# Kernel optimization log

Measured on AMD Instinct MI355X. Metric: run time of the kernel, lower is better.

Reference implementation:

```python
import jax, jax.numpy as jnp
import numpy as np

H = 32        # num query heads
KVH = 8       # num kv heads
D = 128       # head_dim
ROPE_BASE = 10000.0
NEG_INF = jnp.finfo(jnp.float32).min


def rope_interleaved(x):
    """Interleaved (GPT-NeoX-style pairs (x0,x1),(x2,x3),...) RoPE. x: [b,s,h,d]."""
    d = x.shape[-1]
    inv_freq = 1.0 / (ROPE_BASE ** (jnp.arange(0, d, 2, dtype=jnp.float32) / d))  # [d/2]
    pos = jnp.arange(x.shape[1], dtype=jnp.float32)
    ang = pos[:, None] * inv_freq[None, :]                    # [s, d/2]
    cos = jnp.cos(ang)[None, :, None, :]
    sin = jnp.sin(ang)[None, :, None, :]
    xp = x.reshape(*x.shape[:-1], d // 2, 2)
    x1, x2 = xp[..., 0], xp[..., 1]
    r1 = x1 * cos - x2 * sin
    r2 = x1 * sin + x2 * cos
    return jnp.stack([r1, r2], axis=-1).reshape(x.shape)


def setup_inputs() -> dict:
    key = jax.random.key(0)
    k1, k2, k3 = jax.random.split(key, 3)
    B, S, E = 2, 2048, 4096
    x = jax.random.normal(k1, (B, S, E), dtype=jnp.float32)
    wqkv = jax.random.normal(k2, (E + 2 * KVH * D, E), dtype=jnp.float32) * 0.02
    wo = jax.random.normal(k3, (E, E), dtype=jnp.float32) * 0.02
    return {"x": x, "wqkv": wqkv, "wo": wo}


def reference(x, wqkv, wo):
    b, s, e = x.shape
    q_per_kv = H // KVH
    # fused QKV projection (torch Linear layout: y = x @ W.T)
    qkv = jnp.einsum('bse,fe->bsf', x, wqkv)
    # rearrange 'b s (h gs d) -> b s h gs d', gs = q_per_kv + 2
    qkv = qkv.reshape(b, s, KVH, q_per_kv + 2, D)
    q = qkv[..., :q_per_kv, :].reshape(b, s, H, D)   # (h gs) -> H query heads
    k = qkv[..., -2, :]                              # [b,s,KVH,D]
    v = qkv[..., -1, :]
    # RoPE (rotary_emb_dim == head_dim, interleaved)
    q = rope_interleaved(q)
    k = rope_interleaved(k)
    # GQA: expand kv heads to match query heads
    k = jnp.repeat(k, q_per_kv, axis=2)              # [b,s,H,D]
    v = jnp.repeat(v, q_per_kv, axis=2)
    scale = D ** -0.5
    scores = jnp.einsum('bqhd,bkhd->bhqk', q, k) * scale
    causal = jnp.tril(jnp.ones((s, s), dtype=bool))
    scores = jnp.where(causal[None, None], scores, NEG_INF)
    attn = jax.nn.softmax(scores, axis=-1)
    ctx = jnp.einsum('bhqk,bkhd->bqhd', attn, v).reshape(b, s, H * D)
    return jnp.einsum('bsf,ef->bse', ctx, wo)
```

## Files before the change

### kernel.cpp

```cpp
#include <hip/hip_runtime.h>
#include <cstdint>

typedef __bf16 bf16;
typedef __bf16 bf16x8 __attribute__((ext_vector_type(8)));
typedef float  f32x4  __attribute__((ext_vector_type(4)));

#define AS1(p) ((__attribute__((address_space(1))) void*)(p))
#define AS3(p) ((__attribute__((address_space(3))) void*)(p))

__device__ __forceinline__ void gload16(const void* g, void* l) {
  __builtin_amdgcn_global_load_lds(AS1(g), AS3(l), 16, 0, 0);
}

constexpr int B_ = 2, S_ = 2048, E_ = 4096, H_ = 32, KVH_ = 8, D_ = 128;
constexpr int QPK_ = H_ / KVH_;
constexpr int F_ = E_ + 2 * KVH_ * D_;
constexpr int M_ = B_ * S_;

__global__ void f2bf_k(const float* __restrict__ in, bf16* __restrict__ out, int n8) {
  int i = blockIdx.x * 256 + threadIdx.x;
  if (i >= n8) return;
  const float4* p = (const float4*)(in + (size_t)i * 8);
  float4 a = p[0], b = p[1];
  bf16x8 o;
  o[0] = (bf16)a.x; o[1] = (bf16)a.y; o[2] = (bf16)a.z; o[3] = (bf16)a.w;
  o[4] = (bf16)b.x; o[5] = (bf16)b.y; o[6] = (bf16)b.z; o[7] = (bf16)b.w;
  *(bf16x8*)(out + (size_t)i * 8) = o;
}

__global__ void rope_table_k(float2* __restrict__ tab) {
  int i = blockIdx.x * 256 + threadIdx.x;
  int s = i >> 6, f = i & 63;
  float inv = powf(10000.0f, -2.0f * (float)f / 128.0f);
  float ang = (float)s * inv;
  tab[i] = make_float2(cosf(ang), sinf(ang));
}

template <typename OutT>
__global__ __launch_bounds__(512, 2)
void gemm256(const bf16* __restrict__ A, const bf16* __restrict__ B,
             OutT* __restrict__ C, int M, int N, int K) {
  __shared__ bf16 As[2][16384];
  __shared__ bf16 Bs[3][16384];
  const int tid = threadIdx.x;
  const int wid = tid >> 6, lane = tid & 63;
  const int l15 = lane & 15, g = lane >> 4;
  const int wr = wid >> 2, wc = wid & 3;
  const int bm = blockIdx.x, bn = blockIdx.y;
  const bf16* Ab = A + (size_t)bm * 256 * K;
  const bf16* Bb = B + (size_t)bn * 256 * K;
  const int nT = K >> 6;
  const int swzr = (l15 & 7) << 4;

  f32x4 acc[8][4];
#pragma unroll
  for (int m = 0; m < 8; ++m)
#pragma unroll
    for (int n = 0; n < 4; ++n) acc[m][n] = (f32x4){0.f, 0.f, 0.f, 0.f};

  auto stgA = [&](int t) {
#pragma unroll
    for (int i = 0; i < 4; ++i) {
      int lb = i * 8192 + wid * 1024 + lane * 16;
      int row = lb >> 7;
      int colb = (lb & 127) ^ ((row & 7) << 4);
      gload16(Ab + (size_t)row * K + t * 64 + (colb >> 1),
              &As[t & 1][(i * 8192 + wid * 1024) >> 1]);
    }
  };
  auto stgB = [&](int t) {
    bf16* dst = &Bs[t % 3][0];
#pragma unroll
    for (int i = 0; i < 4; ++i) {
      int lb = i * 8192 + wid * 1024 + lane * 16;
      int row = lb >> 7;
      int colb = (lb & 127) ^ ((row & 7) << 4);
      gload16(Bb + (size_t)row * K + t * 64 + (colb >> 1),
              dst + ((i * 8192 + wid * 1024) >> 1));
    }
  };

  stgB(0); stgA(0);
  if (nT > 1) { stgB(1); asm volatile("s_waitcnt vmcnt(4)"); }
  else        { asm volatile("s_waitcnt vmcnt(0)"); }
  __builtin_amdgcn_sched_barrier(0);
  __builtin_amdgcn_s_barrier();

  bf16x8 af[8][2], blo[2][2], bhi[2][2];
  for (int t = 0; t < nT; ++t) {
    const bf16* Asc = &As[t & 1][0];
    const bf16* Bsc = &Bs[t % 3][0];
#pragma unroll
    for (int m = 0; m < 8; ++m) {
      int arow = wr * 128 + m * 16 + l15;
#pragma unroll
      for (int ks = 0; ks < 2; ++ks)
        af[m][ks] = *(const bf16x8*)&Asc[(arow << 6) + (((ks * 64 + g * 16) ^ swzr) >> 1)];
    }
#pragma unroll
    for (int n = 0; n < 2; ++n) {
      int brow = wc * 64 + n * 16 + l15;
#pragma unroll
      for (int ks = 0; ks < 2; ++ks)
        blo[n][ks] = *(const bf16x8*)&Bsc[(brow << 6) + (((ks * 64 + g * 16) ^ swzr) >> 1)];
    }
    if (t + 1 < nT) stgA(t + 1);
    __builtin_amdgcn_s_barrier();
    asm volatile("s_waitcnt lgkmcnt(0)");
    __builtin_amdgcn_sched_barrier(0);
    __builtin_amdgcn_s_setprio(1);
#pragma unroll
    for (int ks = 0; ks < 2; ++ks)
#pragma unroll
      for (int m = 0; m < 8; ++m)
#pragma unroll
        for (int n = 0; n < 2; ++n)
          acc[m][n] = __builtin_amdgcn_mfma_f32_16x16x32_bf16(af[m][ks], blo[n][ks], acc[m][n], 0, 0, 0);
    __builtin_amdgcn_s_setprio(0);
    __builtin_amdgcn_s_barrier();
#pragma unroll
    for (int n = 0; n < 2; ++n) {
      int brow = wc * 64 + 32 + n * 16 + l15;
#pragma unroll
      for (int ks = 0; ks < 2; ++ks)
        bhi[n][ks] = *(const bf16x8*)&Bsc[(brow << 6) + (((ks * 64 + g * 16) ^ swzr) >> 1)];
    }
    if (t + 2 < nT) stgB(t + 2);
    __builtin_amdgcn_s_barrier();
    asm volatile("s_waitcnt lgkmcnt(0)");
    __builtin_amdgcn_sched_barrier(0);
    __builtin_amdgcn_s_setprio(1);
#pragma unroll
    for (int ks = 0; ks < 2; ++ks)
#pragma unroll
      for (int m = 0; m < 8; ++m)
#pragma unroll
        for (int n = 0; n < 2; ++n)
          acc[m][2 + n] = __builtin_amdgcn_mfma_f32_16x16x32_bf16(af[m][ks], bhi[n][ks], acc[m][2 + n], 0, 0, 0);
    __builtin_amdgcn_s_setprio(0);
    if (t + 2 < nT)      { asm volatile("s_waitcnt vmcnt(4)"); }
    else if (t + 1 < nT) { asm volatile("s_waitcnt vmcnt(0)"); }
    __builtin_amdgcn_sched_barrier(0);
    __builtin_amdgcn_s_barrier();
  }

#pragma unroll
  for (int m = 0; m < 8; ++m) {
    int row0 = bm * 256 + wr * 128 + m * 16 + g * 4;
#pragma unroll
    for (int ni = 0; ni < 4; ++ni) {
      int col = bn * 256 + wc * 64 + ni * 16 + l15;
      f32x4 v = acc[m][ni];
#pragma unroll
      for (int r = 0; r < 4; ++r)
        C[(size_t)(row0 + r) * N + col] = (OutT)v[r];
    }
  }
}

__global__ void rope_q_k(const bf16* __restrict__ qkv, const float2* __restrict__ tab,
                         bf16* __restrict__ qout) {
  int idx = blockIdx.x * 256 + threadIdx.x;
  int c = idx & 15;
  int h = (idx >> 4) & 31;
  int s = (idx >> 9) & 2047;
  int b = idx >> 20;
  int d0 = c * 8;
  int kvh = h >> 2, j = h & 3;
  const bf16* src = qkv + (size_t)(b * 2048 + s) * F_ + kvh * (QPK_ + 2) * D_ + j * D_ + d0;
  bf16x8 v = *(const bf16x8*)src;
  const float2* tb = tab + s * 64 + (d0 >> 1);
  bf16x8 o;
#pragma unroll
  for (int p = 0; p < 4; ++p) {
    float x0 = (float)v[2 * p], x1 = (float)v[2 * p + 1];
    float2 cs = tb[p];
    o[2 * p]     = (bf16)(x0 * cs.x - x1 * cs.y);
    o[2 * p + 1] = (bf16)(x0 * cs.y + x1 * cs.x);
  }
  *(bf16x8*)(qout + (((size_t)b * 2048 + s) * 32 + h) * 128 + d0) = o;
}

__global__ void rope_k_k(const bf16* __restrict__ qkv, const float2* __restrict__ tab,
                         bf16* __restrict__ kout) {
  int idx = blockIdx.x * 256 + threadIdx.x;
  int c = idx & 15;
  int kvh = (idx >> 4) & 7;
  int s = (idx >> 7) & 2047;
  int b = idx >> 18;
  int d0 = c * 8;
  const bf16* src = qkv + (size_t)(b * 2048 + s) * F_ + kvh * (QPK_ + 2) * D_ + QPK_ * D_ + d0;
  bf16x8 v = *(const bf16x8*)src;
  const float2* tb = tab + s * 64 + (d0 >> 1);
  bf16x8 o;
#pragma unroll
  for (int p = 0; p < 4; ++p) {
    float x0 = (float)v[2 * p], x1 = (float)v[2 * p + 1];
    float2 cs = tb[p];
    o[2 * p]     = (bf16)(x0 * cs.x - x1 * cs.y);
    o[2 * p + 1] = (bf16)(x0 * cs.y + x1 * cs.x);
  }
  *(bf16x8*)(kout + ((size_t)(b * 8 + kvh) * 2048 + s) * 128 + d0) = o;
}

__global__ void vtrans_k(const bf16* __restrict__ qkv, bf16* __restrict__ vt) {
  int bidx = blockIdx.x;
  int st = bidx & 31;
  int dt = (bidx >> 5) & 3;
  int kvh = (bidx >> 7) & 7;
  int b = bidx >> 10;
  __shared__ bf16 tile[64][40];
  int t = threadIdx.x;
  {
    int sl = t >> 2, d0 = (t & 3) * 8;
    bf16x8 v = *(const bf16x8*)(qkv + (size_t)(b * 2048 + st * 64 + sl) * F_ +
                                kvh * (QPK_ + 2) * D_ + (QPK_ + 1) * D_ + dt * 32 + d0);
#pragma unroll
    for (int i = 0; i < 8; ++i) tile[sl][d0 + i] = v[i];
  }
  __syncthreads();
  {
    int dl = t >> 3, s0 = (t & 7) * 8;
    bf16x8 o;
#pragma unroll
    for (int i = 0; i < 8; ++i) o[i] = tile[s0 + i][dl];
    *(bf16x8*)(vt + ((size_t)(b * 8 + kvh) * 128 + dt * 32 + dl) * 2048 + st * 64 + s0) = o;
  }
}

__global__ __launch_bounds__(512, 2)
void attn_k(const bf16* __restrict__ q, const bf16* __restrict__ k,
            const bf16* __restrict__ vt, bf16* __restrict__ ctx) {
  int bid = blockIdx.x;
  bid = (bid & 7) * 64 + (bid >> 3);
  int qp = bid & 7;
  int h = (bid >> 3) & 31;
  int b = bid >> 8;
  int kvh = h >> 2;
  int tid = threadIdx.x, w = tid >> 6, lane = tid & 63;
  int l15 = lane & 15, g = lane >> 4;

  __shared__ bf16 Ks[3][64 * 128];
  __shared__ bf16 Vs[3][128 * 64];
  __shared__ bf16 Plds[8][16 * 80];

  bf16* Pw = &Plds[w][0];
  const float C2 = 0.08838834764831845f * 1.4426950408889634f;
  const float NEG = -3.0e38f;

  const bf16* kb_base = k + (size_t)(b * 8 + kvh) * 2048 * 128;
  const bf16* vt_base = vt + (size_t)(b * 8 + kvh) * 128 * 2048;

  auto stage = [&](int kv0, int buf) {
#pragma unroll
    for (int i = 0; i < 2; ++i) {
      int lt = i * 8192 + tid * 16;
      int row = lt >> 8;
      int ch = (lt >> 4) & 15;
      int srcel = (ch ^ (row & 7)) << 3;
      gload16(kb_base + (size_t)(kv0 + row) * 128 + srcel,
              &Ks[buf][(i * 8192 + w * 1024) >> 1]);
    }
#pragma unroll
    for (int i = 0; i < 2; ++i) {
      int lt = i * 8192 + tid * 16;
      int row = lt >> 7;
      int ch = (lt >> 4) & 7;
      int srcel = (ch ^ (row & 7)) << 3;
      gload16(vt_base + (size_t)row * 2048 + kv0 + srcel,
              &Vs[buf][(i * 8192 + w * 1024) >> 1]);
    }
  };

  const int kxor = (l15 & 7) << 4;

  for (int pass = 0; pass < 2; ++pass) {
    int qt = pass ? (15 - qp) : qp;
    int qrow0 = qt * 128 + w * 16;

    bf16x8 aq[4];
#pragma unroll
    for (int ks = 0; ks < 4; ++ks)
      aq[ks] = *(const bf16x8*)(q + (((size_t)b * 2048 + qrow0 + l15) * 32 + h) * 128 + ks * 32 + g * 8);

    f32x4 acco[8];
#pragma unroll
    for (int n = 0; n < 8; ++n) acco[n] = (f32x4){0.f, 0.f, 0.f, 0.f};
    float m_r[4] = {NEG, NEG, NEG, NEG};
    float l_r[4] = {0.f, 0.f, 0.f, 0.f};

    const int nk = 2 * qt + 2;
    stage(0, 0);
    stage(64, 1);
    asm volatile("s_waitcnt vmcnt(4)");
    __builtin_amdgcn_sched_barrier(0);
    __builtin_amdgcn_s_barrier();

    for (int kt = 0; kt < nk; ++kt) {
      int kv0 = kt * 64;
      int cur = kt % 3;
      if (kt + 2 < nk) stage(kv0 + 128, (kt + 2) % 3);

      if (kv0 <= qrow0 + 15) {
        f32x4 s[4];
#pragma unroll
        for (int n = 0; n < 4; ++n) s[n] = (f32x4){0.f, 0.f, 0.f, 0.f};
#pragma unroll
        for (int ks = 0; ks < 4; ++ks) {
          int off = ((ks * 64 + g * 16) ^ kxor) >> 1;
#pragma unroll
          for (int n = 0; n < 4; ++n) {
            bf16x8 kb = *(const bf16x8*)&Ks[cur][(n * 16 + l15) * 128 + off];
            s[n] = __builtin_amdgcn_mfma_f32_16x16x32_bf16(aq[ks], kb, s[n], 0, 0, 0);
          }
        }
        if (kv0 + 63 > qrow0) {
#pragma unroll
          for (int n = 0; n < 4; ++n)
#pragma unroll
            for (int r = 0; r < 4; ++r) {
              int qg = qrow0 + g * 4 + r;
              int kg = kv0 + n * 16 + l15;
              if (kg > qg) s[n][r] = NEG;
            }
        }
        float fac[4];
#pragma unroll
        for (int r = 0; r < 4; ++r) {
          float mx = fmaxf(fmaxf(s[0][r], s[1][r]), fmaxf(s[2][r], s[3][r]));
#pragma unroll
          for (int off = 1; off < 16; off <<= 1) mx = fmaxf(mx, __shfl_xor(mx, off));
          float mn = fmaxf(m_r[r], mx);
          fac[r] = exp2f((m_r[r] - mn) * C2);
          m_r[r] = mn;
        }
        float psum[4] = {0.f, 0.f, 0.f, 0.f};
#pragma unroll
        for (int n = 0; n < 4; ++n)
#pragma unroll
          for (int r = 0; r < 4; ++r) {
            float p = exp2f((s[n][r] - m_r[r]) * C2);
            psum[r] += p;
            Pw[(g * 4 + r) * 80 + n * 16 + l15] = (bf16)p;
          }
#pragma unroll
        for (int r = 0; r < 4; ++r) {
          float ps = psum[r];
#pragma unroll
          for (int off = 1; off < 16; off <<= 1) ps += __shfl_xor(ps, off);
          l_r[r] = l_r[r] * fac[r] + ps;
        }
#pragma unroll
        for (int n = 0; n < 8; ++n)
#pragma unroll
          for (int r = 0; r < 4; ++r) acco[n][r] *= fac[r];
        __builtin_amdgcn_sched_barrier(0);
        asm volatile("s_waitcnt lgkmcnt(0)");
        __builtin_amdgcn_sched_barrier(0);
#pragma unroll
        for (int ks = 0; ks < 2; ++ks) {
          bf16x8 pa = *(const bf16x8*)&Pw[l15 * 80 + ks * 32 + g * 8];
          int off = ((ks * 64 + g * 16) ^ kxor) >> 1;
#pragma unroll
          for (int n = 0; n < 8; ++n) {
            bf16x8 vb = *(const bf16x8*)&Vs[cur][(n * 16 + l15) * 64 + off];
            acco[n] = __builtin_amdgcn_mfma_f32_16x16x32_bf16(pa, vb, acco[n], 0, 0, 0);
          }
        }
      }

      if (kt + 1 < nk) {
        if (kt + 2 < nk) { asm volatile("s_waitcnt vmcnt(4)"); }
        else             { asm volatile("s_waitcnt vmcnt(0)"); }
        __builtin_amdgcn_sched_barrier(0);
      }
      __builtin_amdgcn_s_barrier();
    }

#pragma unroll
    for (int r = 0; r < 4; ++r) {
      float inv = 1.0f / l_r[r];
      int qg = qrow0 + g * 4 + r;
#pragma unroll
      for (int n = 0; n < 8; ++n)
        ctx[(((size_t)b * 2048 + qg) * 32 + h) * 128 + n * 16 + l15] = (bf16)(acco[n][r] * inv);
    }
  }
}

extern "C" void kernel_launch(void* const* d_in, const int* in_sizes, int n_in,
                              void* d_out, int out_size, void* d_ws, size_t ws_size,
                              hipStream_t stream) {
  const float* x = (const float*)d_in[0];
  const float* wqkv = (const float*)d_in[1];
  const float* wo = (const float*)d_in[2];
  float* out = (float*)d_out;
  char* ws = (char*)d_ws;

  bf16* xbf    = (bf16*)(ws + 0);
  bf16* wqkvbf = (bf16*)(ws + 33554432);
  bf16* qkvbf  = (bf16*)(ws + 83886080);
  bf16* qbuf   = (bf16*)(ws + 134217728);
  bf16* kbuf   = (bf16*)(ws + 167772160);
  bf16* vtbuf  = (bf16*)(ws + 176160768);
  float2* tab  = (float2*)(ws + 184549376);

  f2bf_k<<<8192, 256, 0, stream>>>(x, xbf, M_ * E_ / 8);
  f2bf_k<<<12288, 256, 0, stream>>>(wqkv, wqkvbf, F_ * E_ / 8);
  rope_table_k<<<512, 256, 0, stream>>>(tab);

  gemm256<bf16><<<dim3(M_ / 256, F_ / 256), 512, 0, stream>>>(xbf, wqkvbf, qkvbf, M_, F_, E_);

  rope_q_k<<<8192, 256, 0, stream>>>(qkvbf, tab, qbuf);
  rope_k_k<<<2048, 256, 0, stream>>>(qkvbf, tab, kbuf);
  vtrans_k<<<2048, 256, 0, stream>>>(qkvbf, vtbuf);

  bf16* wobf = qkvbf;
  f2bf_k<<<8192, 256, 0, stream>>>(wo, wobf, E_ * E_ / 8);

  bf16* ctx = xbf;
  attn_k<<<512, 512, 0, stream>>>(qbuf, kbuf, vtbuf, ctx);

  gemm256<float><<<dim3(M_ / 256, E_ / 256), 512, 0, stream>>>(ctx, wobf, out, M_, E_, E_);
}
```

Measured before the change: 593.0 us.

## Fuse Q RoPE into QKV GEMM epilogue and simplify GEMM pipeline barriers

After: 645.9 us. 1.09x slower.

```diff
diff --git a/kernel.cpp b/kernel.cpp
--- a/kernel.cpp
+++ b/kernel.cpp
@@ -36,10 +36,11 @@
   tab[i] = make_float2(cosf(ang), sinf(ang));
 }
 
-template <typename OutT>
+template <bool FUSEQ, typename OutT>
 __global__ __launch_bounds__(512, 2)
 void gemm256(const bf16* __restrict__ A, const bf16* __restrict__ B,
-             OutT* __restrict__ C, int M, int N, int K) {
+             OutT* __restrict__ C, int M, int N, int K,
+             const float2* __restrict__ tab, bf16* __restrict__ qout) {
   __shared__ bf16 As[2][16384];
   __shared__ bf16 Bs[3][16384];
   const int tid = threadIdx.x;
@@ -80,16 +81,18 @@
     }
   };
 
-  stgB(0); stgA(0);
+  stgA(0); stgB(0);
   if (nT > 1) { stgB(1); asm volatile("s_waitcnt vmcnt(4)"); }
   else        { asm volatile("s_waitcnt vmcnt(0)"); }
   __builtin_amdgcn_sched_barrier(0);
   __builtin_amdgcn_s_barrier();
 
-  bf16x8 af[8][2], blo[2][2], bhi[2][2];
   for (int t = 0; t < nT; ++t) {
     const bf16* Asc = &As[t & 1][0];
     const bf16* Bsc = &Bs[t % 3][0];
+    if (t + 1 < nT) stgA(t + 1);
+    if (t + 2 < nT) stgB(t + 2);
+    bf16x8 af[8][2], blo[2][2], bhi[2][2];
 #pragma unroll
     for (int m = 0; m < 8; ++m) {
       int arow = wr * 128 + m * 16 + l15;
@@ -104,11 +107,6 @@
       for (int ks = 0; ks < 2; ++ks)
         blo[n][ks] = *(const bf16x8*)&Bsc[(brow << 6) + (((ks * 64 + g * 16) ^ swzr) >> 1)];
     }
-    if (t + 1 < nT) stgA(t + 1);
-    __builtin_amdgcn_s_barrier();
-    asm volatile("s_waitcnt lgkmcnt(0)");
-    __builtin_amdgcn_sched_barrier(0);
-    __builtin_amdgcn_s_setprio(1);
 #pragma unroll
     for (int ks = 0; ks < 2; ++ks)
 #pragma unroll
@@ -116,8 +114,6 @@
 #pragma unroll
         for (int n = 0; n < 2; ++n)
           acc[m][n] = __builtin_amdgcn_mfma_f32_16x16x32_bf16(af[m][ks], blo[n][ks], acc[m][n], 0, 0, 0);
-    __builtin_amdgcn_s_setprio(0);
-    __builtin_amdgcn_s_barrier();
 #pragma unroll
     for (int n = 0; n < 2; ++n) {
       int brow = wc * 64 + 32 + n * 16 + l15;
@@ -125,11 +121,6 @@
       for (int ks = 0; ks < 2; ++ks)
         bhi[n][ks] = *(const bf16x8*)&Bsc[(brow << 6) + (((ks * 64 + g * 16) ^ swzr) >> 1)];
     }
-    if (t + 2 < nT) stgB(t + 2);
-    __builtin_amdgcn_s_barrier();
-    asm volatile("s_waitcnt lgkmcnt(0)");
-    __builtin_amdgcn_sched_barrier(0);
-    __builtin_amdgcn_s_setprio(1);
 #pragma unroll
     for (int ks = 0; ks < 2; ++ks)
 #pragma unroll
@@ -137,48 +128,54 @@
 #pragma unroll
         for (int n = 0; n < 2; ++n)
           acc[m][2 + n] = __builtin_amdgcn_mfma_f32_16x16x32_bf16(af[m][ks], bhi[n][ks], acc[m][2 + n], 0, 0, 0);
-    __builtin_amdgcn_s_setprio(0);
+    __builtin_amdgcn_sched_barrier(0);
+    asm volatile("s_waitcnt lgkmcnt(0)");
     if (t + 2 < nT)      { asm volatile("s_waitcnt vmcnt(4)"); }
     else if (t + 1 < nT) { asm volatile("s_waitcnt vmcnt(0)"); }
     __builtin_amdgcn_sched_barrier(0);
     __builtin_amdgcn_s_barrier();
   }
 
-#pragma unroll
-  for (int m = 0; m < 8; ++m) {
-    int row0 = bm * 256 + wr * 128 + m * 16 + g * 4;
-#pragma unroll
-    for (int ni = 0; ni < 4; ++ni) {
-      int col = bn * 256 + wc * 64 + ni * 16 + l15;
-      f32x4 v = acc[m][ni];
-#pragma unroll
-      for (int r = 0; r < 4; ++r)
-        C[(size_t)(row0 + r) * N + col] = (OutT)v[r];
-    }
-  }
-}
-
-__global__ void rope_q_k(const bf16* __restrict__ qkv, const float2* __restrict__ tab,
-                         bf16* __restrict__ qout) {
-  int idx = blockIdx.x * 256 + threadIdx.x;
-  int c = idx & 15;
-  int h = (idx >> 4) & 31;
-  int s = (idx >> 9) & 2047;
-  int b = idx >> 20;
-  int d0 = c * 8;
-  int kvh = h >> 2, j = h & 3;
-  const bf16* src = qkv + (size_t)(b * 2048 + s) * F_ + kvh * (QPK_ + 2) * D_ + j * D_ + d0;
-  bf16x8 v = *(const bf16x8*)src;
-  const float2* tb = tab + s * 64 + (d0 >> 1);
-  bf16x8 o;
-#pragma unroll
-  for (int p = 0; p < 4; ++p) {
-    float x0 = (float)v[2 * p], x1 = (float)v[2 * p + 1];
-    float2 cs = tb[p];
-    o[2 * p]     = (bf16)(x0 * cs.x - x1 * cs.y);
-    o[2 * p + 1] = (bf16)(x0 * cs.y + x1 * cs.x);
-  }
-  *(bf16x8*)(qout + (((size_t)b * 2048 + s) * 32 + h) * 128 + d0) = o;
+  if (FUSEQ && (bn % 3) < 2) {
+    const int r3 = bn % 3, kvh = bn / 3;
+#pragma unroll
+    for (int m = 0; m < 8; ++m) {
+      int srow = wr * 128 + m * 16 + g * 4;
+#pragma unroll
+      for (int ni = 0; ni < 4; ++ni) {
+        int colt = wc * 64 + ni * 16 + l15;
+        int hj = r3 * 2 + (colt >> 7);
+        int d = colt & 127;
+        int f = d >> 1;
+        f32x4 v = acc[m][ni];
+        f32x4 vp;
+#pragma unroll
+        for (int r = 0; r < 4; ++r) vp[r] = __shfl_xor(v[r], 1);
+#pragma unroll
+        for (int r = 0; r < 4; ++r) {
+          int grow = bm * 256 + srow + r;
+          int pos = grow & 2047, bb = grow >> 11;
+          float2 cs = tab[pos * 64 + f];
+          float o = (l15 & 1) ? (vp[r] * cs.y + v[r] * cs.x)
+                              : (v[r] * cs.x - vp[r] * cs.y);
+          qout[(((size_t)bb * 2048 + pos) * 32 + kvh * 4 + hj) * 128 + d] = (bf16)o;
+        }
+      }
+    }
+  } else {
+#pragma unroll
+    for (int m = 0; m < 8; ++m) {
+      int row0 = bm * 256 + wr * 128 + m * 16 + g * 4;
+#pragma unroll
+      for (int ni = 0; ni < 4; ++ni) {
+        int col = bn * 256 + wc * 64 + ni * 16 + l15;
+        f32x4 v = acc[m][ni];
+#pragma unroll
+        for (int r = 0; r < 4; ++r)
+          C[(size_t)(row0 + r) * N + col] = (OutT)v[r];
+      }
+    }
+  }
 }
 
 __global__ void rope_k_k(const bf16* __restrict__ qkv, const float2* __restrict__ tab,
@@ -409,9 +406,9 @@
   f2bf_k<<<12288, 256, 0, stream>>>(wqkv, wqkvbf, F_ * E_ / 8);
   rope_table_k<<<512, 256, 0, stream>>>(tab);
 
-  gemm256<bf16><<<dim3(M_ / 256, F_ / 256), 512, 0, stream>>>(xbf, wqkvbf, qkvbf, M_, F_, E_);
-
-  rope_q_k<<<8192, 256, 0, stream>>>(qkvbf, tab, qbuf);
+  gemm256<true, bf16><<<dim3(M_ / 256, F_ / 256), 512, 0, stream>>>(
+      xbf, wqkvbf, qkvbf, M_, F_, E_, tab, qbuf);
+
   rope_k_k<<<2048, 256, 0, stream>>>(qkvbf, tab, kbuf);
   vtrans_k<<<2048, 256, 0, stream>>>(qkvbf, vtbuf);
 
@@ -421,5 +418,6 @@
   bf16* ctx = xbf;
   attn_k<<<512, 512, 0, stream>>>(qbuf, kbuf, vtbuf, ctx);
 
-  gemm256<float><<<dim3(M_ / 256, E_ / 256), 512, 0, stream>>>(ctx, wobf, out, M_, E_, E_);
-}
+  gemm256<false, float><<<dim3(M_ / 256, E_ / 256), 512, 0, stream>>>(
+      ctx, wobf, out, M_, E_, E_, tab, nullptr);
+}
```
